# Kernel tuning notes

Hardware: AMD Instinct MI355X
Metric: run time of the kernel (lower is better)

## Reference

```python
import jax, jax.numpy as jnp
import numpy as np

VOCAB_SIZE = 8192
DIM = 64


def setup_inputs() -> dict:
    key = jax.random.key(0)
    k1, k2 = jax.random.split(key)
    patches = jax.random.normal(k1, (16, 2048, DIM), dtype=jnp.float32)
    vocab = jax.random.normal(k2, (VOCAB_SIZE, DIM), dtype=jnp.float32)
    return {"patches": patches, "vocab": vocab}


def reference(patches, vocab):
    # torch.cdist(patches, vocab) -> [B, N, K] euclidean distances, then argmin over K.
    # argmin is invariant under sqrt, so compare squared distances:
    x2 = jnp.sum(patches * patches, axis=-1, keepdims=True)       # [B, N, 1]
    c2 = jnp.sum(vocab * vocab, axis=-1)                           # [K]
    xc = jnp.einsum("bnd,kd->bnk", patches, vocab)                # [B, N, K]
    d2 = x2 - 2.0 * xc + c2                                        # [B, N, K]
    tokens = jnp.argmin(d2, axis=-1)                               # [B, N] int
    return tokens
```

## Files before the change

### kernel.cpp

```cpp
#include <hip/hip_runtime.h>
#include <float.h>

#define VOCAB 8192
#define DIM 64
#define NQ 32768
#define CHUNK 64
#define THREADS 256

typedef __attribute__((ext_vector_type(8))) _Float16 half8;
typedef __attribute__((ext_vector_type(4))) float f32x4;

#define LO_SCALE 4096.0f
#define LO_INV   2.44140625e-4f

__global__ __launch_bounds__(256) void c2_kernel(const float* __restrict__ vocab,
                                                 float* __restrict__ c2) {
    int c = blockIdx.x * 256 + threadIdx.x;
    const float4* row = (const float4*)(vocab + (size_t)c * DIM);
    float a0 = 0.f, a1 = 0.f, a2 = 0.f, a3 = 0.f;
#pragma unroll
    for (int k = 0; k < DIM / 4; ++k) {
        float4 v = row[k];
        a0 = fmaf(v.x, v.x, a0); a1 = fmaf(v.y, v.y, a1);
        a2 = fmaf(v.z, v.z, a2); a3 = fmaf(v.w, v.w, a3);
    }
    c2[c] = (a0 + a1) + (a2 + a3);
}

__global__ __launch_bounds__(256) void split_kernel(const float* __restrict__ src,
                                                    _Float16* __restrict__ hi,
                                                    _Float16* __restrict__ lo) {
    int t = blockIdx.x * 256 + threadIdx.x;
    const float4* s = (const float4*)(src + (size_t)t * 8);
    float4 f0 = s[0], f1 = s[1];
    float x[8] = {f0.x, f0.y, f0.z, f0.w, f1.x, f1.y, f1.z, f1.w};
    half8 h, l;
#pragma unroll
    for (int j = 0; j < 8; ++j) {
        _Float16 hh = (_Float16)x[j];
        h[j] = hh;
        l[j] = (_Float16)((x[j] - (float)hh) * LO_SCALE);
    }
    *(half8*)(hi + (size_t)t * 8) = h;
    *(half8*)(lo + (size_t)t * 8) = l;
}

__device__ __forceinline__ void gload_lds(const _Float16* g, void* lds_dst) {
    __builtin_amdgcn_global_load_lds(
        (const __attribute__((address_space(1))) void*)g,
        (__attribute__((address_space(3))) void*)lds_dst, 16, 0, 0);
}

template <int NSLICE>
__global__ __launch_bounds__(THREADS, 2)
void argmin_mfma(const float* __restrict__ patches,
                 const _Float16* __restrict__ vhi,
                 const _Float16* __restrict__ vlo,
                 const float* __restrict__ c2g,
                 float* __restrict__ ws_best,
                 int*   __restrict__ ws_idx) {
    constexpr int CSLICE = VOCAB / NSLICE;
    constexpr int NCHUNK = CSLICE / CHUNK;
    __shared__ __align__(16) char smem[2 * 16384];

    const int tid   = threadIdx.x;
    const int lane  = tid & 63;
    const int w     = tid >> 6;
    const int slice = blockIdx.x & (NSLICE - 1);
    const int qg    = blockIdx.x / NSLICE;
    const int qbase = qg * 256 + w * 64;
    const int cbase = slice * CSLICE;

    const int arow = lane & 15;
    const int akc  = lane >> 4;
    half8 Ah[4][2], Al[4][2];
#pragma unroll
    for (int t = 0; t < 4; ++t)
#pragma unroll
        for (int ks = 0; ks < 2; ++ks) {
            const float* p = patches + (size_t)(qbase + t * 16 + arow) * DIM
                           + ks * 32 + akc * 8;
            float4 f0 = *(const float4*)p;
            float4 f1 = *(const float4*)(p + 4);
            float x[8] = {f0.x, f0.y, f0.z, f0.w, f1.x, f1.y, f1.z, f1.w};
            half8 h, l;
#pragma unroll
            for (int j = 0; j < 8; ++j) {
                _Float16 hh = (_Float16)x[j];
                h[j] = hh;
                l[j] = (_Float16)((x[j] - (float)hh) * LO_SCALE);
            }
            Ah[t][ks] = h; Al[t][ks] = l;
        }

    const int s_srcoff = ((lane >> 3) * DIM) + (((lane & 7) ^ (lane >> 3)) * 8);
    const int fr = lane & 15;
    const int fx = fr & 7;
    const int b_off0 = fr * 128 + (((0 * 4 + akc) ^ fx) * 16);
    const int b_off1 = fr * 128 + (((1 * 4 + akc) ^ fx) * 16);

    float best[4][4];
    int   bidx[4][4];
#pragma unroll
    for (int t = 0; t < 4; ++t)
#pragma unroll
        for (int j = 0; j < 4; ++j) { best[t][j] = -FLT_MAX; bidx[t][j] = 0; }

    {
        const size_t crow = (size_t)cbase * DIM;
#pragma unroll
        for (int j = 0; j < 2; ++j) {
            int r0 = (w + 4 * j) * 8;
            gload_lds(vhi + crow + (size_t)r0 * DIM + s_srcoff, smem + r0 * 128);
            gload_lds(vlo + crow + (size_t)r0 * DIM + s_srcoff, smem + 8192 + r0 * 128);
        }
    }
    __syncthreads();

    for (int ch = 0; ch < NCHUNK; ++ch) {
        const int cur = ch & 1;
        if (ch + 1 < NCHUNK) {
            const size_t crow = (size_t)(cbase + (ch + 1) * CHUNK) * DIM;
            char* dst = smem + (cur ^ 1) * 16384;
#pragma unroll
            for (int j = 0; j < 2; ++j) {
                int r0 = (w + 4 * j) * 8;
                gload_lds(vhi + crow + (size_t)r0 * DIM + s_srcoff, dst + r0 * 128);
                gload_lds(vlo + crow + (size_t)r0 * DIM + s_srcoff, dst + 8192 + r0 * 128);
            }
        }
        const char* hib = smem + cur * 16384;
        const char* lob = hib + 8192;
        const int cb = cbase + ch * CHUNK;

#pragma unroll
        for (int nt = 0; nt < 4; ++nt) {
            const int rt = nt * 16;
            half8 Bh0 = *(const half8*)(hib + rt * 128 + b_off0);
            half8 Bh1 = *(const half8*)(hib + rt * 128 + b_off1);
            half8 Bl0 = *(const half8*)(lob + rt * 128 + b_off0);
            half8 Bl1 = *(const half8*)(lob + rt * 128 + b_off1);
            const float c2h = -0.5f * c2g[cb + rt + fr];
            const int  cidx = cb + rt + fr;
#pragma unroll
            for (int t = 0; t < 4; ++t) {
                f32x4 am = {c2h, c2h, c2h, c2h};
                f32x4 al = {0.f, 0.f, 0.f, 0.f};
                am = __builtin_amdgcn_mfma_f32_16x16x32_f16(Ah[t][0], Bh0, am, 0, 0, 0);
                am = __builtin_amdgcn_mfma_f32_16x16x32_f16(Ah[t][1], Bh1, am, 0, 0, 0);
                al = __builtin_amdgcn_mfma_f32_16x16x32_f16(Ah[t][0], Bl0, al, 0, 0, 0);
                al = __builtin_amdgcn_mfma_f32_16x16x32_f16(Ah[t][1], Bl1, al, 0, 0, 0);
                al = __builtin_amdgcn_mfma_f32_16x16x32_f16(Al[t][0], Bh0, al, 0, 0, 0);
                al = __builtin_amdgcn_mfma_f32_16x16x32_f16(Al[t][1], Bh1, al, 0, 0, 0);
#pragma unroll
                for (int j = 0; j < 4; ++j) {
                    float val = fmaf(al[j], LO_INV, am[j]);
                    if (val > best[t][j]) { best[t][j] = val; bidx[t][j] = cidx; }
                }
            }
        }
        __syncthreads();
    }

#pragma unroll
    for (int t = 0; t < 4; ++t)
#pragma unroll
        for (int j = 0; j < 4; ++j) {
            float b = best[t][j]; int bi = bidx[t][j];
#pragma unroll
            for (int d = 1; d < 16; d <<= 1) {
                float ob = __shfl_xor(b, d, 64);
                int   oi = __shfl_xor(bi, d, 64);
                if (ob > b || (ob == b && oi < bi)) { b = ob; bi = oi; }
            }
            best[t][j] = b; bidx[t][j] = bi;
        }

    if ((lane & 15) == 0) {
        const int rg = lane >> 4;
#pragma unroll
        for (int t = 0; t < 4; ++t)
#pragma unroll
            for (int j = 0; j < 4; ++j) {
                int q = qbase + t * 16 + rg * 4 + j;
                ws_best[(size_t)slice * NQ + q] = best[t][j];
                ws_idx [(size_t)slice * NQ + q] = bidx[t][j];
            }
    }
}

template <int NSLICE>
__global__ __launch_bounds__(256) void merge_kernel(const float* __restrict__ ws_best,
                                                    const int* __restrict__ ws_idx,
                                                    int* __restrict__ out) {
    int q = blockIdx.x * 256 + threadIdx.x;
    float b = ws_best[q]; int bi = ws_idx[q];
#pragma unroll
    for (int s = 1; s < NSLICE; ++s) {
        float v = ws_best[(size_t)s * NQ + q];
        int  vi = ws_idx[(size_t)s * NQ + q];
        if (v > b || (v == b && vi < bi)) { b = v; bi = vi; }
    }
    out[q] = bi;
}

extern "C" void kernel_launch(void* const* d_in, const int* in_sizes, int n_in,
                              void* d_out, int out_size, void* d_ws, size_t ws_size,
                              hipStream_t stream) {
    const float* patches = (const float*)d_in[0];
    const float* vocab   = (const float*)d_in[1];
    char* ws = (char*)d_ws;
    float*    c2    = (float*)ws;
    _Float16* vhi   = (_Float16*)(ws + 32768);
    _Float16* vlo   = (_Float16*)(ws + 32768 + 1048576);
    float*    wbest = (float*)(ws + 32768 + 2097152);
    int* out = (int*)d_out;

    c2_kernel   <<<VOCAB / 256, 256, 0, stream>>>(vocab, c2);
    split_kernel<<<(VOCAB * DIM / 8) / 256, 256, 0, stream>>>(vocab, vhi, vlo);

    const size_t base = 32768 + 2097152;
    if (ws_size >= base + (size_t)8 * NQ * 8) {
        int* widx = (int*)(ws + base + (size_t)8 * NQ * 4);
        argmin_mfma<8><<<128 * 8, THREADS, 0, stream>>>(patches, vhi, vlo, c2, wbest, widx);
        merge_kernel<8><<<NQ / 256, 256, 0, stream>>>(wbest, widx, out);
    } else {
        int* widx = (int*)(ws + base + (size_t)4 * NQ * 4);
        argmin_mfma<4><<<128 * 4, THREADS, 0, stream>>>(patches, vhi, vlo, c2, wbest, widx);
        merge_kernel<4><<<NQ / 256, 256, 0, stream>>>(wbest, widx, out);
    }
}
```

Baseline: 118.6 us.

## Load codebook fragments directly from global memory instead of LDS double-buffering

Removes the LDS staging of vocab hi/lo halves (global_load_lds double buffer plus barriers). Each wave now reads its B fragments straight from global memory, relying on L1/L2 caching because all four waves in a block read the same data. The -0.5 scaling of the squared vocab norms moves into c2_kernel. This drops the block-wide syncs and LDS traffic, but each wave now issues its own global loads and loses the explicit prefetch overlap.

```diff
diff --git a/kernel.cpp b/kernel.cpp
--- a/kernel.cpp
+++ b/kernel.cpp
@@ -4,8 +4,8 @@
 #define VOCAB 8192
 #define DIM 64
 #define NQ 32768
-#define CHUNK 64
 #define THREADS 256
+#define QPB 256
 
 typedef __attribute__((ext_vector_type(8))) _Float16 half8;
 typedef __attribute__((ext_vector_type(4))) float f32x4;
@@ -14,7 +14,7 @@
 #define LO_INV   2.44140625e-4f
 
 __global__ __launch_bounds__(256) void c2_kernel(const float* __restrict__ vocab,
-                                                 float* __restrict__ c2) {
+                                                 float* __restrict__ c2h) {
     int c = blockIdx.x * 256 + threadIdx.x;
     const float4* row = (const float4*)(vocab + (size_t)c * DIM);
     float a0 = 0.f, a1 = 0.f, a2 = 0.f, a3 = 0.f;
@@ -24,7 +24,7 @@
         a0 = fmaf(v.x, v.x, a0); a1 = fmaf(v.y, v.y, a1);
         a2 = fmaf(v.z, v.z, a2); a3 = fmaf(v.w, v.w, a3);
     }
-    c2[c] = (a0 + a1) + (a2 + a3);
+    c2h[c] = -0.5f * ((a0 + a1) + (a2 + a3));
 }
 
 __global__ __launch_bounds__(256) void split_kernel(const float* __restrict__ src,
@@ -45,12 +45,6 @@
     *(half8*)(lo + (size_t)t * 8) = l;
 }
 
-__device__ __forceinline__ void gload_lds(const _Float16* g, void* lds_dst) {
-    __builtin_amdgcn_global_load_lds(
-        (const __attribute__((address_space(1))) void*)g,
-        (__attribute__((address_space(3))) void*)lds_dst, 16, 0, 0);
-}
-
 template <int NSLICE>
 __global__ __launch_bounds__(THREADS, 2)
 void argmin_mfma(const float* __restrict__ patches,
@@ -60,15 +54,11 @@
                  float* __restrict__ ws_best,
                  int*   __restrict__ ws_idx) {
     constexpr int CSLICE = VOCAB / NSLICE;
-    constexpr int NCHUNK = CSLICE / CHUNK;
-    __shared__ __align__(16) char smem[2 * 16384];
-
-    const int tid   = threadIdx.x;
-    const int lane  = tid & 63;
-    const int w     = tid >> 6;
+    const int lane  = threadIdx.x & 63;
+    const int w     = threadIdx.x >> 6;
     const int slice = blockIdx.x & (NSLICE - 1);
     const int qg    = blockIdx.x / NSLICE;
-    const int qbase = qg * 256 + w * 64;
+    const int qbase = qg * QPB + w * 64;
     const int cbase = slice * CSLICE;
 
     const int arow = lane & 15;
@@ -93,11 +83,10 @@
             Ah[t][ks] = h; Al[t][ks] = l;
         }
 
-    const int s_srcoff = ((lane >> 3) * DIM) + (((lane & 7) ^ (lane >> 3)) * 8);
-    const int fr = lane & 15;
-    const int fx = fr & 7;
-    const int b_off0 = fr * 128 + (((0 * 4 + akc) ^ fx) * 16);
-    const int b_off1 = fr * 128 + (((1 * 4 + akc) ^ fx) * 16);
+    const int  fr   = lane & 15;
+    const int  boff = fr * 128 + akc * 16;
+    const char* hptr = (const char*)vhi + (size_t)cbase * 128 + boff;
+    const char* lptr = (const char*)vlo + (size_t)cbase * 128 + boff;
 
     float best[4][4];
     int   bidx[4][4];
@@ -106,60 +95,32 @@
 #pragma unroll
         for (int j = 0; j < 4; ++j) { best[t][j] = -FLT_MAX; bidx[t][j] = 0; }
 
-    {
-        const size_t crow = (size_t)cbase * DIM;
+#pragma unroll 2
+    for (int ct = 0; ct < CSLICE / 16; ++ct) {
+        const char* hb = hptr + (size_t)ct * 2048;
+        const char* lb = lptr + (size_t)ct * 2048;
+        half8 Bh0 = *(const half8*)(hb);
+        half8 Bh1 = *(const half8*)(hb + 64);
+        half8 Bl0 = *(const half8*)(lb);
+        half8 Bl1 = *(const half8*)(lb + 64);
+        const int   cidx = cbase + ct * 16 + fr;
+        const float c2h  = c2g[cidx];
 #pragma unroll
-        for (int j = 0; j < 2; ++j) {
-            int r0 = (w + 4 * j) * 8;
-            gload_lds(vhi + crow + (size_t)r0 * DIM + s_srcoff, smem + r0 * 128);
-            gload_lds(vlo + crow + (size_t)r0 * DIM + s_srcoff, smem + 8192 + r0 * 128);
-        }
-    }
-    __syncthreads();
-
-    for (int ch = 0; ch < NCHUNK; ++ch) {
-        const int cur = ch & 1;
-        if (ch + 1 < NCHUNK) {
-            const size_t crow = (size_t)(cbase + (ch + 1) * CHUNK) * DIM;
-            char* dst = smem + (cur ^ 1) * 16384;
+        for (int t = 0; t < 4; ++t) {
+            f32x4 am = {c2h, c2h, c2h, c2h};
+            f32x4 al = {0.f, 0.f, 0.f, 0.f};
+            am = __builtin_amdgcn_mfma_f32_16x16x32_f16(Ah[t][0], Bh0, am, 0, 0, 0);
+            am = __builtin_amdgcn_mfma_f32_16x16x32_f16(Ah[t][1], Bh1, am, 0, 0, 0);
+            al = __builtin_amdgcn_mfma_f32_16x16x32_f16(Ah[t][0], Bl0, al, 0, 0, 0);
+            al = __builtin_amdgcn_mfma_f32_16x16x32_f16(Ah[t][1], Bl1, al, 0, 0, 0);
+            al = __builtin_amdgcn_mfma_f32_16x16x32_f16(Al[t][0], Bh0, al, 0, 0, 0);
+            al = __builtin_amdgcn_mfma_f32_16x16x32_f16(Al[t][1], Bh1, al, 0, 0, 0);
 #pragma unroll
-            for (int j = 0; j < 2; ++j) {
-                int r0 = (w + 4 * j) * 8;
-                gload_lds(vhi + crow + (size_t)r0 * DIM + s_srcoff, dst + r0 * 128);
-                gload_lds(vlo + crow + (size_t)r0 * DIM + s_srcoff, dst + 8192 + r0 * 128);
+            for (int j = 0; j < 4; ++j) {
+                float val = fmaf(al[j], LO_INV, am[j]);
+                if (val > best[t][j]) { best[t][j] = val; bidx[t][j] = cidx; }
             }
         }
-        const char* hib = smem + cur * 16384;
-        const char* lob = hib + 8192;
-        const int cb = cbase + ch * CHUNK;
-
-#pragma unroll
-        for (int nt = 0; nt < 4; ++nt) {
-            const int rt = nt * 16;
-            half8 Bh0 = *(const half8*)(hib + rt * 128 + b_off0);
-            half8 Bh1 = *(const half8*)(hib + rt * 128 + b_off1);
-            half8 Bl0 = *(const half8*)(lob + rt * 128 + b_off0);
-            half8 Bl1 = *(const half8*)(lob + rt * 128 + b_off1);
-            const float c2h = -0.5f * c2g[cb + rt + fr];
-            const int  cidx = cb + rt + fr;
-#pragma unroll
-            for (int t = 0; t < 4; ++t) {
-                f32x4 am = {c2h, c2h, c2h, c2h};
-                f32x4 al = {0.f, 0.f, 0.f, 0.f};
-                am = __builtin_amdgcn_mfma_f32_16x16x32_f16(Ah[t][0], Bh0, am, 0, 0, 0);
-                am = __builtin_amdgcn_mfma_f32_16x16x32_f16(Ah[t][1], Bh1, am, 0, 0, 0);
-                al = __builtin_amdgcn_mfma_f32_16x16x32_f16(Ah[t][0], Bl0, al, 0, 0, 0);
-                al = __builtin_amdgcn_mfma_f32_16x16x32_f16(Ah[t][1], Bl1, al, 0, 0, 0);
-                al = __builtin_amdgcn_mfma_f32_16x16x32_f16(Al[t][0], Bh0, al, 0, 0, 0);
-                al = __builtin_amdgcn_mfma_f32_16x16x32_f16(Al[t][1], Bh1, al, 0, 0, 0);
-#pragma unroll
-                for (int j = 0; j < 4; ++j) {
-                    float val = fmaf(al[j], LO_INV, am[j]);
-                    if (val > best[t][j]) { best[t][j] = val; bidx[t][j] = cidx; }
-                }
-            }
-        }
-        __syncthreads();
     }
 
 #pragma unroll
@@ -222,11 +183,11 @@
     const size_t base = 32768 + 2097152;
     if (ws_size >= base + (size_t)8 * NQ * 8) {
         int* widx = (int*)(ws + base + (size_t)8 * NQ * 4);
-        argmin_mfma<8><<<128 * 8, THREADS, 0, stream>>>(patches, vhi, vlo, c2, wbest, widx);
+        argmin_mfma<8><<<(NQ / QPB) * 8, THREADS, 0, stream>>>(patches, vhi, vlo, c2, wbest, widx);
         merge_kernel<8><<<NQ / 256, 256, 0, stream>>>(wbest, widx, out);
     } else {
         int* widx = (int*)(ws + base + (size_t)4 * NQ * 4);
-        argmin_mfma<4><<<128 * 4, THREADS, 0, stream>>>(patches, vhi, vlo, c2, wbest, widx);
+        argmin_mfma<4><<<(NQ / QPB) * 4, THREADS, 0, stream>>>(patches, vhi, vlo, c2, wbest, widx);
         merge_kernel<4><<<NQ / 256, 256, 0, stream>>>(wbest, widx, out);
     }
 }
```

After: 183.8 us. 54.9% more time.
